# Kernel tuning notes

Measured on AMD Instinct MI355X. Metric: run time of the kernel, lower is better.

## Reference

```python
import jax, jax.numpy as jnp
import numpy as np

N = 50000
E = 800000
HIGH, LOW, EMB = 128, 32, 64
HID, HEADS, OUT = 32, 8, 8
IN1 = HIGH + EMB  # 192
IN2 = HID * HEADS  # 256
NEG_SLOPE = 0.2


def setup_inputs() -> dict:
    key = jax.random.key(0)
    ks = jax.random.split(key, 12)
    s = lambda k, shape: (jax.random.normal(k, shape, dtype=jnp.float32) * 0.1)
    return {
        "high_dim_features": jax.random.normal(ks[0], (N, HIGH), dtype=jnp.float32),
        "low_dim_features": jax.random.normal(ks[1], (N, LOW), dtype=jnp.float32),
        "edge_index": jax.random.randint(ks[2], (2, E), 0, N, dtype=jnp.int32),
        "W_emb": s(ks[3], (LOW, EMB)),
        "b_emb": jnp.zeros((EMB,), jnp.float32),
        "W1": s(ks[4], (IN1, HEADS * HID)),
        "att_src1": s(ks[5], (HEADS, HID)),
        "att_dst1": s(ks[6], (HEADS, HID)),
        "b1": jnp.zeros((HEADS * HID,), jnp.float32),
        "W2": s(ks[7], (IN2, OUT)),
        "att_src2": s(ks[8], (1, OUT)),
        "att_dst2": s(ks[9], (1, OUT)),
        "b2": jnp.zeros((OUT,), jnp.float32),
    }


def _gat_layer(x, src, dst, W, att_src, att_dst, bias, heads, out_ch, concat):
    # x: [N, F_in]; src/dst: [E'] (self-loops already appended)
    n = x.shape[0]
    h = (x @ W).reshape(n, heads, out_ch)            # [N, H, C]
    a_src = jnp.einsum('nhc,hc->nh', h, att_src)     # [N, H]
    a_dst = jnp.einsum('nhc,hc->nh', h, att_dst)
    alpha = a_src[src] + a_dst[dst]                  # [E', H]
    alpha = jax.nn.leaky_relu(alpha, NEG_SLOPE)
    # segment softmax over incoming edges per destination node
    m = jax.ops.segment_max(alpha, dst, num_segments=n)
    ea = jnp.exp(alpha - m[dst])
    z = jax.ops.segment_sum(ea, dst, num_segments=n)
    alpha = ea / (z[dst] + 1e-16)                    # [E', H]
    msg = h[src] * alpha[:, :, None]                 # [E', H, C]
    out = jax.ops.segment_sum(msg, dst, num_segments=n)  # [N, H, C]
    if concat:
        out = out.reshape(n, heads * out_ch)
    else:
        out = out.mean(axis=1)
    return out + bias


def reference(high_dim_features, low_dim_features, edge_index,
              W_emb, b_emb, W1, att_src1, att_dst1, b1,
              W2, att_src2, att_dst2, b2):
    # embedding + elu, concat
    emb = jax.nn.elu(low_dim_features @ W_emb + b_emb)
    x = jnp.concatenate([high_dim_features, emb], axis=1)  # [N, IN1]
    # add self-loops (PyG default)
    loops = jnp.arange(N, dtype=edge_index.dtype)
    src = jnp.concatenate([edge_index[0], loops])
    dst = jnp.concatenate([edge_index[1], loops])
    x = _gat_layer(x, src, dst, W1, att_src1, att_dst1, b1, HEADS, HID, True)
    x = jax.nn.elu(x)  # dropout: eval mode no-op
    x = _gat_layer(x, src, dst, W2, att_src2, att_dst2, b2, 1, OUT, False)
    return jax.nn.log_softmax(x, axis=1)
```

## Files before the change

kernel.cpp:

```cpp
#include <hip/hip_runtime.h>
#include <hip/hip_bf16.h>

typedef __hip_bfloat16 bf16;
typedef short bf16x8 __attribute__((ext_vector_type(8)));
typedef float f32x4  __attribute__((ext_vector_type(4)));

__device__ __forceinline__ float bf2f(bf16 v){ return __bfloat162float(v); }
__device__ __forceinline__ bf16  f2bf(float f){ return __float2bfloat16(f); }
__device__ __forceinline__ float lrelu(float a){ return a > 0.f ? a : 0.2f*a; }
__device__ __forceinline__ float bfbits(short s){
    union{unsigned u; float f;} cv; cv.u = ((unsigned)(unsigned short)s) << 16; return cv.f;
}
__device__ __forceinline__ short bf16s(float f){ bf16 q = f2bf(f); return *(short*)&q; }
__device__ __forceinline__ float cvtf(const void* p, int i, int isb){
    return isb ? bf2f(((const bf16*)p)[i]) : ((const float*)p)[i];
}
__device__ __forceinline__ short cvts(const void* p, int i, int isb){
    return isb ? ((const short*)p)[i] : bf16s(((const float*)p)[i]);
}
__device__ __forceinline__ bf16x8 load8(const void* base, size_t off, int isb){
    if (isb) return *(const bf16x8*)((const bf16*)base + off);
    const float* f = (const float*)base + off;
    f32x4 v0 = *(const f32x4*)f;
    f32x4 v1 = *(const f32x4*)(f + 4);
    short r[8];
    #pragma unroll
    for (int j = 0; j < 4; j++) r[j]   = bf16s(v0[j]);
    #pragma unroll
    for (int j = 0; j < 4; j++) r[4+j] = bf16s(v1[j]);
    return *(const bf16x8*)r;
}

__global__ void k_init(const unsigned short* __restrict__ raw, int* __restrict__ flag,
        int* __restrict__ counts, int N){
    int t = threadIdx.x;
    int i = blockIdx.x*256 + t;
    if (i < N) counts[i] = 1;
    if (blockIdx.x == 0){
        unsigned short w = raw[2*t];
        int e = (w >> 7) & 0xFF;
        int ok = (e >= 90 && e <= 140) ? 1 : 0;
        __shared__ int cnt;
        if (t == 0) cnt = 0;
        __syncthreads();
        atomicAdd(&cnt, ok);
        __syncthreads();
        if (t == 0) *flag = (cnt >= 192) ? 1 : 0;
    }
}

__global__ __launch_bounds__(256) void k_prep(const void* __restrict__ low,
        const void* __restrict__ Wemb, const void* __restrict__ bemb,
        const void* __restrict__ W1, const void* __restrict__ W2,
        bf16* __restrict__ emb, bf16* __restrict__ Bp, bf16* __restrict__ Bp2,
        const int* __restrict__ ei, int* __restrict__ counts,
        const int* __restrict__ flag, int N, int E, int nEmb, int nPack, int nCnt){
    __shared__ float wem[2048 + 64];
    __shared__ short lows[1024];
    int t = threadIdx.x;
    int b = blockIdx.x;
    int isb = *flag;
    if (b >= nEmb + nPack){
        int cb = b - nEmb - nPack;
        for (int i = cb*256 + t; i < E; i += nCnt*256){
            atomicAdd(&counts[ei[E + i]], 1);
        }
        return;
    }
    if (b >= nEmb){
        int i = (b - nEmb)*256 + t;
        if (i < 16*6*64*8){
            int j = i & 7;
            int lane = (i >> 3) & 63;
            int r = i >> 9;
            int kt = r % 6, nt = r / 6;
            int k = kt*32 + (lane >> 4)*8 + j;
            int n = nt*16 + (lane & 15);
            *(short*)&Bp[i] = cvts(W1, k*256 + n, isb);
        } else {
            int i2 = i - 16*6*64*8;
            if (i2 >= 8*64*8) return;
            int j = i2 & 7;
            int lane = (i2 >> 3) & 63;
            int kt = i2 >> 9;
            int k = kt*32 + (lane >> 4)*8 + j;
            int n = lane & 15;
            *(short*)&Bp2[i2] = (n < 8) ? cvts(W2, k*8 + n, isb) : (short)0;
        }
        return;
    }
    int nb0 = b * 32;
    for (int i = t; i < 2048; i += 256) wem[i] = cvtf(Wemb, i, isb);
    if (t < 64) wem[2048 + t] = cvtf(bemb, t, isb);
    int lim = (N - nb0) * 32; if (lim > 1024) lim = 1024;
    for (int i = t; i < 1024; i += 256)
        lows[i] = (i < lim) ? cvts(low, nb0*32 + i, isb) : (short)0;
    __syncthreads();
    int nl = t >> 3, j8 = (t & 7) * 8;
    float acc[8];
    #pragma unroll
    for (int j = 0; j < 8; j++) acc[j] = wem[2048 + j8 + j];
    for (int k = 0; k < 32; k++){
        float lv = bfbits(lows[nl*32 + k]);
        f32x4 w0 = *(const f32x4*)&wem[k*64 + j8];
        f32x4 w1 = *(const f32x4*)&wem[k*64 + j8 + 4];
        #pragma unroll
        for (int j = 0; j < 4; j++) acc[j]   += lv * w0[j];
        #pragma unroll
        for (int j = 0; j < 4; j++) acc[4+j] += lv * w1[j];
    }
    int n = nb0 + nl;
    if (n < N){
        short ov[8];
        #pragma unroll
        for (int j = 0; j < 8; j++){
            float v = acc[j];
            ov[j] = bf16s(v > 0.f ? v : expm1f(v));
        }
        *(bf16x8*)&emb[(size_t)n*64 + j8] = *(const bf16x8*)ov;
    }
}

__global__ __launch_bounds__(256) void k_scan_local(const int* __restrict__ counts,
        int* __restrict__ rowptr, int* __restrict__ partials, int N){
    __shared__ int sd[256];
    int t = threadIdx.x;
    int i = blockIdx.x*256 + t;
    int v = (i < N) ? counts[i] : 0;
    sd[t] = v;
    __syncthreads();
    #pragma unroll
    for (int off = 1; off < 256; off <<= 1){
        int a = (t >= off) ? sd[t - off] : 0;
        __syncthreads();
        sd[t] += a;
        __syncthreads();
    }
    if (i < N) rowptr[i] = sd[t] - v;
    if (t == 255) partials[blockIdx.x] = sd[255];
}

__global__ __launch_bounds__(256) void k_scan_fin(const int* __restrict__ partials,
        int* __restrict__ rowptr, int* __restrict__ cursor, int* __restrict__ srcs,
        int N, int NB){
    __shared__ int sd[256];
    int b = blockIdx.x, t = threadIdx.x;
    int off = 0, total = 0;
    for (int base = 0; base < NB; base += 256){
        int v = (base + t < NB) ? partials[base + t] : 0;
        __syncthreads();
        sd[t] = v;
        __syncthreads();
        #pragma unroll
        for (int o2 = 1; o2 < 256; o2 <<= 1){
            int a = (t >= o2) ? sd[t - o2] : 0;
            __syncthreads();
            sd[t] += a;
            __syncthreads();
        }
        if (b >= base && b < base + 256){
            int idx = b - base;
            int local = (idx == 0) ? 0 : sd[idx - 1];
            off = total + local;
        }
        total += sd[255];
    }
    int i = b*256 + t;
    if (i < N){
        int r = rowptr[i] + off;
        rowptr[i] = r;
        srcs[r]   = i;
        cursor[i] = r + 1;
    }
    if (b == NB-1 && t == 255) rowptr[N] = total;
}

__global__ __launch_bounds__(256, 3) void k_sg(
        const int* __restrict__ ei, int* __restrict__ cursor, int* __restrict__ srcs,
        const void* __restrict__ highv, const bf16* __restrict__ emb,
        const bf16* __restrict__ Bp, const void* __restrict__ attS,
        const void* __restrict__ attD, bf16* __restrict__ h1,
        float* __restrict__ a_s, float* __restrict__ a_d,
        const int* __restrict__ flag, int N, int E, int nG){
    const int RS = 260;
    __shared__ float eb[16*260 + 16];
    __shared__ float att[512];
    int t = threadIdx.x;
    if ((int)blockIdx.x >= nG){
        int i = (blockIdx.x - nG)*256 + t;
        if (i < E){
            int src = ei[i];
            int dst = ei[E + i];
            int pos = atomicAdd(&cursor[dst], 1);
            srcs[pos] = src;
        }
        return;
    }
    int isb = *flag;
    att[t] = cvtf(attS, t, isb);
    att[256 + t] = cvtf(attD, t, isb);
    int w = t >> 6, lane = t & 63;
    int m_lo = lane & 15, quad = lane >> 4;
    int m0 = blockIdx.x * 64;
    int mr[4];
    #pragma unroll
    for (int rt = 0; rt < 4; rt++){
        int m = m0 + rt*16 + m_lo;
        mr[rt] = m < N ? m : N-1;
    }
    f32x4 acc[4][4];
    #pragma unroll
    for (int rt = 0; rt < 4; rt++)
        #pragma unroll
        for (int ct = 0; ct < 4; ct++) acc[rt][ct] = (f32x4){0.f,0.f,0.f,0.f};

    #pragma unroll 2
    for (int kt = 0; kt < 6; kt++){
        bf16x8 a[4], b[4];
        if (kt < 4){
            #pragma unroll
            for (int rt = 0; rt < 4; rt++)
                a[rt] = load8(highv, (size_t)mr[rt]*128 + kt*32 + quad*8, isb);
        } else {
            #pragma unroll
            for (int rt = 0; rt < 4; rt++)
                a[rt] = *(const bf16x8*)&emb[(size_t)mr[rt]*64 + (kt-4)*32 + quad*8];
        }
        #pragma unroll
        for (int ct = 0; ct < 4; ct++)
            b[ct] = *(const bf16x8*)&Bp[(size_t)(((w*4 + ct)*6 + kt)*64 + lane)*8];
        #pragma unroll
        for (int rt = 0; rt < 4; rt++)
            #pragma unroll
            for (int ct = 0; ct < 4; ct++)
                acc[rt][ct] = __builtin_amdgcn_mfma_f32_16x16x32_bf16(a[rt], b[ct], acc[rt][ct], 0, 0, 0);
    }

    #pragma unroll 1
    for (int rt = 0; rt < 4; rt++){
        __syncthreads();
        #pragma unroll
        for (int ct = 0; ct < 4; ct++)
            #pragma unroll
            for (int reg = 0; reg < 4; reg++)
                eb[(quad*4 + reg)*RS + w*64 + ct*16 + m_lo] = acc[rt][ct][reg];
        __syncthreads();
        int r = t >> 4, cb = t & 15;
        int c0 = cb * 16;
        int m = m0 + rt*16 + r;
        f32x4 v[4];
        #pragma unroll
        for (int p = 0; p < 4; p++) v[p] = *(const f32x4*)&eb[r*RS + c0 + p*4];
        float ps = 0.f, pd = 0.f;
        #pragma unroll
        for (int p = 0; p < 4; p++)
            #pragma unroll
            for (int j = 0; j < 4; j++){
                ps += v[p][j] * att[c0 + p*4 + j];
                pd += v[p][j] * att[256 + c0 + p*4 + j];
            }
        if (m < N){
            short ov[16];
            #pragma unroll
            for (int p = 0; p < 4; p++)
                #pragma unroll
                for (int j = 0; j < 4; j++) ov[p*4+j] = bf16s(v[p][j]);
            *(bf16x8*)&h1[(size_t)m*256 + c0]     = *(const bf16x8*)&ov[0];
            *(bf16x8*)&h1[(size_t)m*256 + c0 + 8] = *(const bf16x8*)&ov[8];
        }
        ps += __shfl_xor(ps, 1);
        pd += __shfl_xor(pd, 1);
        if (((t & 1) == 0) && m < N){
            int hd = cb >> 1;
            a_s[m*8 + hd] = ps;
            a_d[m*8 + hd] = pd;
        }
    }
}

__global__ __launch_bounds__(256) void k_edge1(const int* __restrict__ rowptr,
        const int* __restrict__ srcs, const float* __restrict__ a_s,
        const float* __restrict__ a_d, const bf16* __restrict__ h1,
        const void* __restrict__ b1, bf16* __restrict__ x2,
        const int* __restrict__ flag, int N){
    int t = threadIdx.x;
    int lane = t & 63, wv = t >> 6;
    int n = blockIdx.x*4 + wv;
    if (n >= N) return;
    int beg = rowptr[n];
    int deg = rowptr[n+1] - beg;

    int cl = lane & 31;
    int hb = cl >> 2;
    int half = lane >> 5;
    float adb = a_d[n*8 + hb];

    float acc[8];
    #pragma unroll
    for (int j = 0; j < 8; j++) acc[j] = 0.f;
    float z = 0.f;

    int e = half;
    for (; e + 6 < deg; e += 8){
        int s0 = srcs[beg + e];
        int s1 = srcs[beg + e + 2];
        int s2 = srcs[beg + e + 4];
        int s3 = srcs[beg + e + 6];
        float w0 = __expf(fminf(lrelu(a_s[s0*8 + hb] + adb), 80.f));
        float w1 = __expf(fminf(lrelu(a_s[s1*8 + hb] + adb), 80.f));
        float w2 = __expf(fminf(lrelu(a_s[s2*8 + hb] + adb), 80.f));
        float w3 = __expf(fminf(lrelu(a_s[s3*8 + hb] + adb), 80.f));
        bf16x8 v0 = *(const bf16x8*)&h1[(size_t)s0*256 + cl*8];
        bf16x8 v1 = *(const bf16x8*)&h1[(size_t)s1*256 + cl*8];
        bf16x8 v2 = *(const bf16x8*)&h1[(size_t)s2*256 + cl*8];
        bf16x8 v3 = *(const bf16x8*)&h1[(size_t)s3*256 + cl*8];
        z += (w0 + w1) + (w2 + w3);
        #pragma unroll
        for (int j = 0; j < 8; j++) acc[j] += w0 * bfbits(v0[j]);
        #pragma unroll
        for (int j = 0; j < 8; j++) acc[j] += w1 * bfbits(v1[j]);
        #pragma unroll
        for (int j = 0; j < 8; j++) acc[j] += w2 * bfbits(v2[j]);
        #pragma unroll
        for (int j = 0; j < 8; j++) acc[j] += w3 * bfbits(v3[j]);
    }
    for (; e < deg; e += 2){
        int s = srcs[beg + e];
        float w = __expf(fminf(lrelu(a_s[s*8 + hb] + adb), 80.f));
        bf16x8 hv = *(const bf16x8*)&h1[(size_t)s*256 + cl*8];
        z += w;
        #pragma unroll
        for (int j = 0; j < 8; j++) acc[j] += w * bfbits(hv[j]);
    }
    #pragma unroll
    for (int j = 0; j < 8; j++) acc[j] += __shfl_xor(acc[j], 32);
    z += __shfl_xor(z, 32);
    float rz = 1.f / (z + 1e-16f);

    if (half == 0){
        int isb = *flag;
        bf16x8 bv = load8(b1, cl*8, isb);
        short ov[8];
        #pragma unroll
        for (int j = 0; j < 8; j++){
            float v = acc[j] * rz + bfbits(bv[j]);
            ov[j] = bf16s(v > 0.f ? v : expm1f(v));
        }
        *(bf16x8*)&x2[(size_t)n*256 + cl*8] = *(const bf16x8*)ov;
    }
}

__global__ __launch_bounds__(256) void k_gemm2(const bf16* __restrict__ x2,
        const bf16* __restrict__ Bp2, const void* __restrict__ attS,
        const void* __restrict__ attD, float* __restrict__ h2,
        float* __restrict__ a2s, float* __restrict__ a2d,
        const int* __restrict__ flag, int N){
    int t = threadIdx.x;
    int isb = *flag;
    int w = t >> 6, lane = t & 63;
    int m_lo = lane & 15, quad = lane >> 4;
    int m0 = blockIdx.x*64 + w*16;
    int mr = m0 + m_lo; if (mr >= N) mr = N-1;
    f32x4 acc = (f32x4){0.f,0.f,0.f,0.f};
    #pragma unroll
    for (int kt = 0; kt < 8; kt++){
        bf16x8 a = *(const bf16x8*)&x2[(size_t)mr*256 + kt*32 + quad*8];
        bf16x8 b = *(const bf16x8*)&Bp2[(size_t)(kt*64 + lane)*8];
        acc = __builtin_amdgcn_mfma_f32_16x16x32_bf16(a, b, acc, 0, 0, 0);
    }
    float s2 = (m_lo < 8) ? cvtf(attS, m_lo, isb) : 0.f;
    float d2 = (m_lo < 8) ? cvtf(attD, m_lo, isb) : 0.f;
    #pragma unroll
    for (int reg = 0; reg < 4; reg++){
        int m = m0 + quad*4 + reg;
        float val = acc[reg];
        float ps = val * s2, pd = val * d2;
        ps += __shfl_xor(ps, 1); ps += __shfl_xor(ps, 2);
        ps += __shfl_xor(ps, 4); ps += __shfl_xor(ps, 8);
        pd += __shfl_xor(pd, 1); pd += __shfl_xor(pd, 2);
        pd += __shfl_xor(pd, 4); pd += __shfl_xor(pd, 8);
        if (m < N){
            if (m_lo < 8) h2[(size_t)m*8 + m_lo] = val;
            if (m_lo == 0){ a2s[m] = ps; a2d[m] = pd; }
        }
    }
}

__global__ __launch_bounds__(256) void k_edge2(const int* __restrict__ rowptr,
        const int* __restrict__ srcs, const float* __restrict__ a2s,
        const float* __restrict__ a2d, const float* __restrict__ h2,
        const void* __restrict__ b2, void* __restrict__ outv,
        const int* __restrict__ flag, int N){
    int t = threadIdx.x;
    int lane = t & 63, wv = t >> 6;
    int n = blockIdx.x*4 + wv;
    if (n >= N) return;
    int beg = rowptr[n];
    int deg = rowptr[n+1] - beg;
    float adh = a2d[n];
    int ep = lane >> 3, c = lane & 7;
    float acc = 0.f, z = 0.f;
    for (int e = ep; e < deg; e += 8){
        int s = srcs[beg + e];
        float w = __expf(fminf(lrelu(a2s[s] + adh), 80.f));
        z += w;
        acc += w * h2[(size_t)s*8 + c];
    }
    acc += __shfl_xor(acc, 8);
    acc += __shfl_xor(acc, 16);
    acc += __shfl_xor(acc, 32);
    z += __shfl_xor(z, 8);
    z += __shfl_xor(z, 16);
    z += __shfl_xor(z, 32);
    int isb = *flag;
    float val = acc / (z + 1e-16f) + cvtf(b2, c, isb);
    float mx = val;
    mx = fmaxf(mx, __shfl_xor(mx, 1));
    mx = fmaxf(mx, __shfl_xor(mx, 2));
    mx = fmaxf(mx, __shfl_xor(mx, 4));
    float se = __expf(val - mx);
    se += __shfl_xor(se, 1); se += __shfl_xor(se, 2); se += __shfl_xor(se, 4);
    float r = val - mx - __logf(se);
    if (lane < 8){
        if (isb) ((bf16*)outv)[(size_t)n*8 + c] = f2bf(r);
        else     ((float*)outv)[(size_t)n*8 + c] = r;
    }
}

extern "C" void kernel_launch(void* const* d_in, const int* in_sizes, int n_in,
                              void* d_out, int out_size, void* d_ws, size_t ws_size,
                              hipStream_t stream) {
    const int* ei = (const int*)d_in[2];
    const int N = in_sizes[0] / 128;
    const int E = in_sizes[2] / 2;
    const int ET = E + N;
    const int NB = (N + 255) / 256;

    char* p = (char*)d_ws;
    auto alloc = [&](size_t bytes) -> void* {
        char* r = p;
        p += (bytes + 255) & ~(size_t)255;
        return (void*)r;
    };
    int*   flag     = (int*)  alloc(256);
    int*   counts   = (int*)  alloc((size_t)N*4);
    int*   rowptr   = (int*)  alloc((size_t)(N+1)*4);
    int*   cursor   = (int*)  alloc((size_t)N*4);
    int*   srcs     = (int*)  alloc((size_t)ET*4);
    int*   partials = (int*)  alloc((size_t)NB*4);
    bf16*  Bp       = (bf16*) alloc((size_t)192*256*2);
    bf16*  Bp2      = (bf16*) alloc((size_t)8*64*8*2);
    bf16*  emb      = (bf16*) alloc((size_t)N*64*2);
    bf16*  h1       = (bf16*) alloc((size_t)N*256*2);
    float* a_s      = (float*)alloc((size_t)N*8*4);
    float* a_d      = (float*)alloc((size_t)N*8*4);
    bf16*  x2       = (bf16*) alloc((size_t)N*256*2);
    float* h2       = (float*)alloc((size_t)N*8*4);
    float* a2s      = (float*)alloc((size_t)N*4);
    float* a2d      = (float*)alloc((size_t)N*4);

    k_init<<<NB, 256, 0, stream>>>((const unsigned short*)d_in[0], flag, counts, N);

    {
        int nEmb  = (N + 31)/32;
        int nPack = (16*6*64*8 + 8*64*8 + 255)/256;
        int nCnt  = 1024;
        k_prep<<<nEmb + nPack + nCnt, 256, 0, stream>>>(d_in[1], d_in[3], d_in[4],
                d_in[5], d_in[9], emb, Bp, Bp2, ei, counts, flag, N, E, nEmb, nPack, nCnt);
    }
    k_scan_local<<<NB, 256, 0, stream>>>(counts, rowptr, partials, N);
    k_scan_fin  <<<NB, 256, 0, stream>>>(partials, rowptr, cursor, srcs, N, NB);
    {
        int nG = (N + 63)/64;
        int nScat = (E + 255)/256;
        k_sg<<<nG + nScat, 256, 0, stream>>>(ei, cursor, srcs,
                d_in[0], emb, Bp, d_in[6], d_in[7], h1, a_s, a_d, flag, N, E, nG);
    }
    k_edge1<<<(N + 3)/4, 256, 0, stream>>>(rowptr, srcs, a_s, a_d, h1, d_in[8], x2, flag, N);
    k_gemm2<<<(N + 63)/64, 256, 0, stream>>>(x2, Bp2, d_in[10], d_in[11], h2, a2s, a2d, flag, N);
    k_edge2<<<(N + 3)/4, 256, 0, stream>>>(rowptr, srcs, a2s, a2d, h2, d_in[12], d_out, flag, N);
}
```

Before: 368.7 us.

## Replace per-node global-atomic CSR build with two-level bucketed counting sort

Builds the destination-sorted CSR with a two-level radix approach: a coarse histogram over 256-node buckets using shared-memory atomics, a single-block bucket scan, a chunked scatter that packs the low dst byte with the src index, and a per-bucket fine pass that computes rowptr and places sources using shared atomics. This replaces per-edge global atomics on N counters and cursors, and drops the two-kernel global scan. It adds an intermediate packed array and an extra kernel, and assumes src fits in 24 bits and that there are at most 256 buckets (N ≤ 65536).

New measurement: 313.4 us. -15.0%, faster.

```diff
diff --git a/kernel.cpp b/kernel.cpp
--- a/kernel.cpp
+++ b/kernel.cpp
@@ -4,6 +4,8 @@
 typedef __hip_bfloat16 bf16;
 typedef short bf16x8 __attribute__((ext_vector_type(8)));
 typedef float f32x4  __attribute__((ext_vector_type(4)));
+
+#define CHK 8192
 
 __device__ __forceinline__ float bf2f(bf16 v){ return __bfloat162float(v); }
 __device__ __forceinline__ bf16  f2bf(float f){ return __float2bfloat16(f); }
@@ -31,11 +33,11 @@
     return *(const bf16x8*)r;
 }
 
-__global__ void k_init(const unsigned short* __restrict__ raw, int* __restrict__ flag,
-        int* __restrict__ counts, int N){
-    int t = threadIdx.x;
-    int i = blockIdx.x*256 + t;
-    if (i < N) counts[i] = 1;
+__global__ __launch_bounds__(256) void k_init(const unsigned short* __restrict__ raw,
+        int* __restrict__ flag, const int* __restrict__ dst,
+        int* __restrict__ bucketCnt, int E, int NBUK, int nBlk){
+    __shared__ int h[256];
+    int t = threadIdx.x;
     if (blockIdx.x == 0){
         unsigned short w = raw[2*t];
         int e = (w >> 7) & 0xFF;
@@ -47,26 +49,24 @@
         __syncthreads();
         if (t == 0) *flag = (cnt >= 192) ? 1 : 0;
     }
+    h[t] = 0;
+    __syncthreads();
+    for (int i = blockIdx.x*256 + t; i < E; i += nBlk*256)
+        atomicAdd(&h[((unsigned)dst[i]) >> 8], 1);
+    __syncthreads();
+    if (t < NBUK && h[t]) atomicAdd(&bucketCnt[t], h[t]);
 }
 
 __global__ __launch_bounds__(256) void k_prep(const void* __restrict__ low,
         const void* __restrict__ Wemb, const void* __restrict__ bemb,
         const void* __restrict__ W1, const void* __restrict__ W2,
         bf16* __restrict__ emb, bf16* __restrict__ Bp, bf16* __restrict__ Bp2,
-        const int* __restrict__ ei, int* __restrict__ counts,
-        const int* __restrict__ flag, int N, int E, int nEmb, int nPack, int nCnt){
+        const int* __restrict__ flag, int N, int nEmb){
     __shared__ float wem[2048 + 64];
     __shared__ short lows[1024];
     int t = threadIdx.x;
     int b = blockIdx.x;
     int isb = *flag;
-    if (b >= nEmb + nPack){
-        int cb = b - nEmb - nPack;
-        for (int i = cb*256 + t; i < E; i += nCnt*256){
-            atomicAdd(&counts[ei[E + i]], 1);
-        }
-        return;
-    }
     if (b >= nEmb){
         int i = (b - nEmb)*256 + t;
         if (i < 16*6*64*8){
@@ -121,12 +121,12 @@
     }
 }
 
-__global__ __launch_bounds__(256) void k_scan_local(const int* __restrict__ counts,
-        int* __restrict__ rowptr, int* __restrict__ partials, int N){
+__global__ __launch_bounds__(256) void k_bscan(const int* __restrict__ bucketCnt,
+        int* __restrict__ bucketPtr, int* __restrict__ bucketCur,
+        int* __restrict__ rowptr, int N, int E, int NBUK){
     __shared__ int sd[256];
     int t = threadIdx.x;
-    int i = blockIdx.x*256 + t;
-    int v = (i < N) ? counts[i] : 0;
+    int v = (t < NBUK) ? bucketCnt[t] : 0;
     sd[t] = v;
     __syncthreads();
     #pragma unroll
@@ -136,66 +136,52 @@
         sd[t] += a;
         __syncthreads();
     }
-    if (i < N) rowptr[i] = sd[t] - v;
-    if (t == 255) partials[blockIdx.x] = sd[255];
-}
-
-__global__ __launch_bounds__(256) void k_scan_fin(const int* __restrict__ partials,
-        int* __restrict__ rowptr, int* __restrict__ cursor, int* __restrict__ srcs,
-        int N, int NB){
-    __shared__ int sd[256];
-    int b = blockIdx.x, t = threadIdx.x;
-    int off = 0, total = 0;
-    for (int base = 0; base < NB; base += 256){
-        int v = (base + t < NB) ? partials[base + t] : 0;
-        __syncthreads();
-        sd[t] = v;
-        __syncthreads();
-        #pragma unroll
-        for (int o2 = 1; o2 < 256; o2 <<= 1){
-            int a = (t >= o2) ? sd[t - o2] : 0;
-            __syncthreads();
-            sd[t] += a;
-            __syncthreads();
-        }
-        if (b >= base && b < base + 256){
-            int idx = b - base;
-            int local = (idx == 0) ? 0 : sd[idx - 1];
-            off = total + local;
-        }
-        total += sd[255];
-    }
-    int i = b*256 + t;
-    if (i < N){
-        int r = rowptr[i] + off;
-        rowptr[i] = r;
-        srcs[r]   = i;
-        cursor[i] = r + 1;
-    }
-    if (b == NB-1 && t == 255) rowptr[N] = total;
+    int excl = sd[t] - v;
+    if (t < NBUK){ bucketPtr[t] = excl; bucketCur[t] = excl; }
+    if (t == 0){ bucketPtr[NBUK] = sd[255]; rowptr[N] = E + N; }
 }
 
 __global__ __launch_bounds__(256, 3) void k_sg(
-        const int* __restrict__ ei, int* __restrict__ cursor, int* __restrict__ srcs,
+        const int* __restrict__ ei, int* __restrict__ bucketCur, int* __restrict__ pk,
         const void* __restrict__ highv, const bf16* __restrict__ emb,
         const bf16* __restrict__ Bp, const void* __restrict__ attS,
         const void* __restrict__ attD, bf16* __restrict__ h1,
         float* __restrict__ a_s, float* __restrict__ a_d,
-        const int* __restrict__ flag, int N, int E, int nG){
+        const int* __restrict__ flag, int N, int E, int nG, int NBUK){
     const int RS = 260;
-    __shared__ float eb[16*260 + 16];
-    __shared__ float att[512];
+    __shared__ union SM {
+        struct { float eb[16*260 + 16]; float att[512]; } g;
+        struct { unsigned short dstS[CHK]; int hist[256]; int cur[256]; } s;
+    } sm;
     int t = threadIdx.x;
     if ((int)blockIdx.x >= nG){
-        int i = (blockIdx.x - nG)*256 + t;
-        if (i < E){
-            int src = ei[i];
-            int dst = ei[E + i];
-            int pos = atomicAdd(&cursor[dst], 1);
-            srcs[pos] = src;
+        int cb = blockIdx.x - nG;
+        int base = cb * CHK;
+        int cnt = E - base; if (cnt > CHK) cnt = CHK;
+        sm.s.hist[t] = 0;
+        __syncthreads();
+        const int* dstp = ei + E + base;
+        for (int i = t; i < cnt; i += 256){
+            int d = dstp[i];
+            sm.s.dstS[i] = (unsigned short)d;
+            atomicAdd(&sm.s.hist[((unsigned)d) >> 8], 1);
+        }
+        __syncthreads();
+        if (t < NBUK){
+            int c = sm.s.hist[t];
+            sm.s.cur[t] = c ? atomicAdd(&bucketCur[t], c) : 0;
+        }
+        __syncthreads();
+        const int* srcp = ei + base;
+        for (int i = t; i < cnt; i += 256){
+            int d = sm.s.dstS[i];
+            int pos = atomicAdd(&sm.s.cur[d >> 8], 1);
+            pk[pos] = ((d & 255) << 24) | srcp[i];
         }
         return;
     }
+    float* eb  = sm.g.eb;
+    float* att = sm.g.att;
     int isb = *flag;
     att[t] = cvtf(attS, t, isb);
     att[256 + t] = cvtf(attD, t, isb);
@@ -275,6 +261,45 @@
             a_s[m*8 + hd] = ps;
             a_d[m*8 + hd] = pd;
         }
+    }
+}
+
+__global__ __launch_bounds__(256) void k_fine(const int* __restrict__ bucketPtr,
+        const int* __restrict__ pk, int* __restrict__ rowptr, int* __restrict__ srcs,
+        int N){
+    __shared__ int cnt[256];
+    __shared__ int sd[256];
+    int t = threadIdx.x;
+    int b = blockIdx.x;
+    int d0 = b << 8;
+    int nd = N - d0; if (nd > 256) nd = 256;
+    int ebeg = bucketPtr[b], eend = bucketPtr[b+1];
+    cnt[t] = (t < nd) ? 1 : 0;
+    __syncthreads();
+    for (int i = ebeg + t; i < eend; i += 256)
+        atomicAdd(&cnt[((unsigned)pk[i]) >> 24], 1);
+    __syncthreads();
+    int v = cnt[t];
+    sd[t] = v;
+    __syncthreads();
+    #pragma unroll
+    for (int off = 1; off < 256; off <<= 1){
+        int a = (t >= off) ? sd[t - off] : 0;
+        __syncthreads();
+        sd[t] += a;
+        __syncthreads();
+    }
+    int r = ebeg + d0 + sd[t] - v;
+    if (t < nd){
+        rowptr[d0 + t] = r;
+        srcs[r] = d0 + t;
+        cnt[t] = r + 1;
+    }
+    __syncthreads();
+    for (int i = ebeg + t; i < eend; i += 256){
+        int p = pk[i];
+        int pos = atomicAdd(&cnt[((unsigned)p) >> 24], 1);
+        srcs[pos] = p & 0xFFFFFF;
     }
 }
 
@@ -434,7 +459,7 @@
     const int N = in_sizes[0] / 128;
     const int E = in_sizes[2] / 2;
     const int ET = E + N;
-    const int NB = (N + 255) / 256;
+    const int NBUK = (N + 255) >> 8;
 
     char* p = (char*)d_ws;
     auto alloc = [&](size_t bytes) -> void* {
@@ -442,40 +467,41 @@
         p += (bytes + 255) & ~(size_t)255;
         return (void*)r;
     };
-    int*   flag     = (int*)  alloc(256);
-    int*   counts   = (int*)  alloc((size_t)N*4);
-    int*   rowptr   = (int*)  alloc((size_t)(N+1)*4);
-    int*   cursor   = (int*)  alloc((size_t)N*4);
-    int*   srcs     = (int*)  alloc((size_t)ET*4);
-    int*   partials = (int*)  alloc((size_t)NB*4);
-    bf16*  Bp       = (bf16*) alloc((size_t)192*256*2);
-    bf16*  Bp2      = (bf16*) alloc((size_t)8*64*8*2);
-    bf16*  emb      = (bf16*) alloc((size_t)N*64*2);
-    bf16*  h1       = (bf16*) alloc((size_t)N*256*2);
-    float* a_s      = (float*)alloc((size_t)N*8*4);
-    float* a_d      = (float*)alloc((size_t)N*8*4);
-    bf16*  x2       = (bf16*) alloc((size_t)N*256*2);
-    float* h2       = (float*)alloc((size_t)N*8*4);
-    float* a2s      = (float*)alloc((size_t)N*4);
-    float* a2d      = (float*)alloc((size_t)N*4);
-
-    k_init<<<NB, 256, 0, stream>>>((const unsigned short*)d_in[0], flag, counts, N);
-
+    int*   flag      = (int*)  alloc(256);
+    int*   bucketCnt = (int*)  alloc((size_t)NBUK*4);
+    int*   bucketPtr = (int*)  alloc((size_t)(NBUK+1)*4);
+    int*   bucketCur = (int*)  alloc((size_t)NBUK*4);
+    int*   rowptr    = (int*)  alloc((size_t)(N+1)*4);
+    int*   srcs      = (int*)  alloc((size_t)ET*4);
+    int*   pk        = (int*)  alloc((size_t)E*4);
+    bf16*  Bp        = (bf16*) alloc((size_t)192*256*2);
+    bf16*  Bp2       = (bf16*) alloc((size_t)8*64*8*2);
+    bf16*  emb       = (bf16*) alloc((size_t)N*64*2);
+    bf16*  h1        = (bf16*) alloc((size_t)N*256*2);
+    float* a_s       = (float*)alloc((size_t)N*8*4);
+    float* a_d       = (float*)alloc((size_t)N*8*4);
+    bf16*  x2        = (bf16*) alloc((size_t)N*256*2);
+    float* h2        = (float*)alloc((size_t)N*8*4);
+    float* a2s       = (float*)alloc((size_t)N*4);
+    float* a2d       = (float*)alloc((size_t)N*4);
+
+    hipMemsetAsync(bucketCnt, 0, (size_t)NBUK*4, stream);
+    k_init<<<256, 256, 0, stream>>>((const unsigned short*)d_in[0], flag,
+            ei + E, bucketCnt, E, NBUK, 256);
     {
         int nEmb  = (N + 31)/32;
         int nPack = (16*6*64*8 + 8*64*8 + 255)/256;
-        int nCnt  = 1024;
-        k_prep<<<nEmb + nPack + nCnt, 256, 0, stream>>>(d_in[1], d_in[3], d_in[4],
-                d_in[5], d_in[9], emb, Bp, Bp2, ei, counts, flag, N, E, nEmb, nPack, nCnt);
-    }
-    k_scan_local<<<NB, 256, 0, stream>>>(counts, rowptr, partials, N);
-    k_scan_fin  <<<NB, 256, 0, stream>>>(partials, rowptr, cursor, srcs, N, NB);
+        k_prep<<<nEmb + nPack, 256, 0, stream>>>(d_in[1], d_in[3], d_in[4],
+                d_in[5], d_in[9], emb, Bp, Bp2, flag, N, nEmb);
+    }
+    k_bscan<<<1, 256, 0, stream>>>(bucketCnt, bucketPtr, bucketCur, rowptr, N, E, NBUK);
     {
         int nG = (N + 63)/64;
-        int nScat = (E + 255)/256;
-        k_sg<<<nG + nScat, 256, 0, stream>>>(ei, cursor, srcs,
-                d_in[0], emb, Bp, d_in[6], d_in[7], h1, a_s, a_d, flag, N, E, nG);
-    }
+        int nScat = (E + CHK - 1)/CHK;
+        k_sg<<<nG + nScat, 256, 0, stream>>>(ei, bucketCur, pk,
+                d_in[0], emb, Bp, d_in[6], d_in[7], h1, a_s, a_d, flag, N, E, nG, NBUK);
+    }
+    k_fine<<<NBUK, 256, 0, stream>>>(bucketPtr, pk, rowptr, srcs, N);
     k_edge1<<<(N + 3)/4, 256, 0, stream>>>(rowptr, srcs, a_s, a_d, h1, d_in[8], x2, flag, N);
     k_gemm2<<<(N + 63)/64, 256, 0, stream>>>(x2, Bp2, d_in[10], d_in[11], h2, a2s, a2d, flag, N);
     k_edge2<<<(N + 3)/4, 256, 0, stream>>>(rowptr, srcs, a2s, a2d, h2, d_in[12], d_out, flag, N);
```
